# Kernel tuning notes

Measured on AMD Instinct MI355X. Metric: run time of the kernel, lower is better.

## Reference

```python
import jax, jax.numpy as jnp
import numpy as np

N = 200000          # nodes
E = 6400000         # edges (before self-loops)
L = 4               # layer_n
H = 9               # hidden_channels (hardcoded in module)
G = 2000            # graphs in batch
C = 2               # num_classes
NEG_SLOPE = 0.2     # GATConv default leaky_relu slope for attention logits


def setup_inputs() -> dict:
    key = jax.random.key(0)
    ks = jax.random.split(key, 9)
    x = jax.random.normal(ks[0], (N, H), dtype=jnp.float32)
    edge_index = jax.random.randint(ks[1], (2, E), 0, N, dtype=jnp.int32)
    batch = jnp.sort(jax.random.randint(ks[2], (N,), 0, G, dtype=jnp.int32))
    W = jax.random.normal(ks[3], (L, H, H), dtype=jnp.float32) * 0.3
    att_src = jax.random.normal(ks[4], (L, H), dtype=jnp.float32) * 0.3
    att_dst = jax.random.normal(ks[5], (L, H), dtype=jnp.float32) * 0.3
    bias = jax.random.normal(ks[6], (L, H), dtype=jnp.float32) * 0.1
    fc_w = jax.random.normal(ks[7], (L * H, C), dtype=jnp.float32) * 0.2
    fc_b = jax.random.normal(ks[8], (C,), dtype=jnp.float32) * 0.1
    return dict(x=x, edge_index=edge_index, batch=batch, W=W,
                att_src=att_src, att_dst=att_dst, bias=bias,
                fc_w=fc_w, fc_b=fc_b)


def _gat_layer(x, W_l, a_src, a_dst, b_l, src, dst, n):
    # h: [N, H] transformed features (linear, no bias per PyG default)
    h = x @ W_l
    alpha_s = h @ a_src            # [N]
    alpha_d = h @ a_dst            # [N]
    # attention logits per edge (src -> dst), GAT softmax grouped by dst
    e = jax.nn.leaky_relu(alpha_s[src] + alpha_d[dst], NEG_SLOPE)  # [E']
    e = e - jax.ops.segment_max(e, dst, num_segments=n)[dst]
    w = jnp.exp(e)
    denom = jax.ops.segment_sum(w, dst, num_segments=n)[dst]
    alpha = w / denom              # [E']
    out = jax.ops.segment_sum(alpha[:, None] * h[src], dst, num_segments=n)
    return out + b_l


def reference(x, edge_index, batch, W, att_src, att_dst, bias, fc_w, fc_b):
    n = x.shape[0]
    loops = jnp.arange(n, dtype=edge_index.dtype)
    src = jnp.concatenate([edge_index[0], loops])  # add_self_loops=True
    dst = jnp.concatenate([edge_index[1], loops])
    jk = []
    h = x
    for l in range(L):
        h = _gat_layer(h, W[l], att_src[l], att_dst[l], bias[l], src, dst, n)
        h = jax.nn.relu(h)
        jk.append(h)
    jk = jnp.concatenate(jk, axis=1)               # [N, L*H]
    pooled = jax.ops.segment_max(jk, batch, num_segments=G)
    pooled = jnp.where(jnp.isfinite(pooled), pooled, 0.0)  # guard empty graphs
    # dropout is identity at inference
    return pooled @ fc_w + fc_b
```

## Files before the change

### kernel.cpp

```cpp
#include <hip/hip_runtime.h>
#include <hip/hip_fp16.h>

#define Nn 200000
#define Ee 6400000
#define EP 6600000
#define Hh 9
#define Ll 4
#define Gg 2000
#define Cc 2
#define JK 36
#define NCB ((Nn + 1023) >> 10)
#define EPB 8192
#define NBLKA ((EP + EPB - 1) / EPB)
#define NB ((Nn + 255) / 256)
#define NPB 32
#define NAB (Nn / NPB)
#define CAP 3072
#define CAPB 36864
#define HTS (NCB + 1)
#define HALF_N (Nn / 2)

union H2F { __half2 h; float f; };


__global__ __launch_bounds__(256) void kA_scatter(
    const int* __restrict__ src, const int* __restrict__ dst,
    int* __restrict__ ctot, int* __restrict__ histT,
    unsigned* __restrict__ bucketed)
{
    __shared__ unsigned pbuf[EPB];
    __shared__ int lh[NCB];
    __shared__ int s[256];
    int t = threadIdx.x;
    if (t < NCB) lh[t] = 0;
    __syncthreads();
    const int base = blockIdx.x * EPB;
    const int nseg = min(EPB, EP - base);
    for (int j = t; j < nseg; j += 256) {
        int e = base + j;
        int d = (e < Ee) ? dst[e] : (e - Ee);
        atomicAdd(&lh[d >> 10], 1);
    }
    __syncthreads();
    int v = (t < NCB) ? lh[t] : 0;
    s[t] = v; __syncthreads();
    for (int off = 1; off < 256; off <<= 1) {
        int u = (t >= off) ? s[t - off] : 0;
        __syncthreads();
        s[t] += u;
        __syncthreads();
    }
    int* hrow = histT + (size_t)blockIdx.x * HTS;
    if (t < NCB) {
        int ex = s[t] - v;
        lh[t] = ex;
        hrow[t] = ex;
        if (v) atomicAdd(&ctot[t], v);
    }
    if (t == 0) hrow[NCB] = nseg;
    __syncthreads();
    for (int j = t; j < nseg; j += 256) {
        int e = base + j;
        int sv, d;
        if (e < Ee) { sv = src[e]; d = dst[e]; } else { sv = e - Ee; d = sv; }
        int pos = atomicAdd(&lh[d >> 10], 1);
        unsigned p = (unsigned)sv | ((unsigned)(d & 1023) << 18);
        if (sv >= HALF_N) p |= (1u << 28);
        pbuf[pos] = p;
    }
    __syncthreads();
    for (int j = t; j < nseg; j += 256)
        bucketed[base + j] = pbuf[j];
}

__global__ __launch_bounds__(256) void k_scan(
    const int* __restrict__ ctot, int* __restrict__ cbase,
    int* __restrict__ row_ptr)
{
    __shared__ int s[256];
    int t = threadIdx.x;
    int v = (t < NCB) ? ctot[t] : 0;
    s[t] = v; __syncthreads();
    for (int off = 1; off < 256; off <<= 1) {
        int u = (t >= off) ? s[t - off] : 0;
        __syncthreads();
        s[t] += u;
        __syncthreads();
    }
    if (t < NCB) cbase[t] = s[t] - v;
    if (t == 0) { cbase[NCB] = EP; row_ptr[Nn] = EP; }
}

__global__ __launch_bounds__(1024) void kB_csr(
    const unsigned* __restrict__ bucketed, const int* __restrict__ histT,
    const int* __restrict__ cbase, int* __restrict__ row_ptr,
    int* __restrict__ csr_src)
{
    __shared__ int2 hb[NBLKA];
    __shared__ int bh[2048];
    __shared__ unsigned pbuf[CAPB];
    __shared__ int wsum[16];
    const int k = blockIdx.x;
    const int t = threadIdx.x;
    const int w = t >> 6, lane = t & 63;
    bh[t] = 0; bh[t + 1024] = 0;
    for (int j = t; j < NBLKA; j += 1024) {
        const int* hrow = histT + (size_t)j * HTS + k;
        hb[j] = make_int2(hrow[0], hrow[1]);
    }
    __syncthreads();
    for (int b = w; b < NBLKA; b += 16 * 4) {
        int2 es[4]; unsigned ps[4];
#pragma unroll
        for (int u = 0; u < 4; ++u) {
            int bb = b + 16 * u;
            int2 e = (bb < NBLKA) ? hb[bb] : make_int2(0, 0);
            es[u] = e;
            int j = e.x + lane;
            ps[u] = (j < e.y)
                ? __builtin_nontemporal_load(bucketed + (size_t)bb * EPB + j)
                : 0u;
        }
#pragma unroll
        for (int u = 0; u < 4; ++u) {
            int bb = b + 16 * u;
            if (bb >= NBLKA) break;
            int j = es[u].x + lane;
            if (j < es[u].y) {
                unsigned p = ps[u];
                atomicAdd(&bh[(((p >> 18) & 1023) << 1) | ((p >> 28) & 1)], 1);
            }
            for (j += 64; j < es[u].y; j += 64) {
                unsigned p = __builtin_nontemporal_load(
                    bucketed + (size_t)bb * EPB + j);
                atomicAdd(&bh[(((p >> 18) & 1023) << 1) | ((p >> 28) & 1)], 1);
            }
        }
    }
    __syncthreads();
    int v0 = bh[2 * t], v1 = bh[2 * t + 1];
    int sum = v0 + v1;
    int incl = sum;
#pragma unroll
    for (int off = 1; off < 64; off <<= 1) {
        int u = __shfl_up(incl, off);
        if (lane >= off) incl += u;
    }
    if (lane == 63) wsum[w] = incl;
    __syncthreads();
    if (t == 0) {
        int acc = 0;
#pragma unroll
        for (int i2 = 0; i2 < 16; ++i2) { int x = wsum[i2]; wsum[i2] = acc; acc += x; }
    }
    __syncthreads();
    int excl = wsum[w] + incl - sum;
    const int base_k = cbase[k];
    const int nseg_b = cbase[k + 1] - base_k;
    const int node = (k << 10) + t;
    if (node < Nn) row_ptr[node] = base_k + excl;
    bh[2 * t] = excl;
    bh[2 * t + 1] = excl + v0;
    __syncthreads();
    const bool fit = (nseg_b <= CAPB);
    if (fit) {
        for (int b = w; b < NBLKA; b += 16 * 4) {
            int2 es[4]; unsigned ps[4];
#pragma unroll
            for (int u = 0; u < 4; ++u) {
                int bb = b + 16 * u;
                int2 e = (bb < NBLKA) ? hb[bb] : make_int2(0, 0);
                es[u] = e;
                int j = e.x + lane;
                ps[u] = (j < e.y)
                    ? __builtin_nontemporal_load(bucketed + (size_t)bb * EPB + j)
                    : 0u;
            }
#pragma unroll
            for (int u = 0; u < 4; ++u) {
                int bb = b + 16 * u;
                if (bb >= NBLKA) break;
                int j = es[u].x + lane;
                if (j < es[u].y) {
                    unsigned p = ps[u];
                    int pos = atomicAdd(
                        &bh[(((p >> 18) & 1023) << 1) | ((p >> 28) & 1)], 1);
                    pbuf[pos] = p & 0x3FFFFu;
                }
                for (j += 64; j < es[u].y; j += 64) {
                    unsigned p = __builtin_nontemporal_load(
                        bucketed + (size_t)bb * EPB + j);
                    int pos = atomicAdd(
                        &bh[(((p >> 18) & 1023) << 1) | ((p >> 28) & 1)], 1);
                    pbuf[pos] = p & 0x3FFFFu;
                }
            }
        }
        __syncthreads();
        for (int j = t; j < nseg_b; j += 1024)
            csr_src[base_k + j] = (int)pbuf[j];
    } else {
        for (int b = w; b < NBLKA; b += 16) {
            int2 e = hb[b];
            int rb = b * EPB;
            for (int j = e.x + lane; j < e.y; j += 64) {
                unsigned p = bucketed[rb + j];
                int pos = base_k + atomicAdd(
                    &bh[(((p >> 18) & 1023) << 1) | ((p >> 28) & 1)], 1);
                csr_src[pos] = (int)(p & 0x3FFFFu);
            }
        }
    }
}


__global__ __launch_bounds__(256) void k_transform(
    const float* __restrict__ xin, int xstride,
    const float* __restrict__ Wl,
    const float* __restrict__ adst,
    char* __restrict__ P)
{
    int i = blockIdx.x * blockDim.x + threadIdx.x;
    if (i >= Nn) return;
    const float* xp = xin + (size_t)i * xstride;
    float xi[Hh];
#pragma unroll
    for (int k = 0; k < Hh; ++k) xi[k] = xp[k];
    float hv[Hh];
#pragma unroll
    for (int j = 0; j < Hh; ++j) {
        float s = 0.f;
#pragma unroll
        for (int k = 0; k < Hh; ++k) s += xi[k] * Wl[k * Hh + j];
        hv[j] = s;
    }
    float ad = 0.f;
#pragma unroll
    for (int j = 0; j < Hh; ++j) ad += hv[j] * adst[j];
    H2F u01, u23, u45, u67;
    u01.h = __floats2half2_rn(hv[0], hv[1]);
    u23.h = __floats2half2_rn(hv[2], hv[3]);
    u45.h = __floats2half2_rn(hv[4], hv[5]);
    u67.h = __floats2half2_rn(hv[6], hv[7]);
    char* rp = P + ((size_t)i << 5);
    *(float4*)rp        = make_float4(u01.f, u23.f, u45.f, u67.f);
    *(float2*)(rp + 16) = make_float2(hv[8], ad);
}

#define AGG_EDGE(F, X8)                                                     \
    {                                                                       \
        H2F u; float2 p;                                                    \
        u.f = (F).x; p = __half22float2(u.h); float x0 = p.x, x1 = p.y;     \
        u.f = (F).y; p = __half22float2(u.h); float x2 = p.x, x3 = p.y;     \
        u.f = (F).z; p = __half22float2(u.h); float x4 = p.x, x5 = p.y;     \
        u.f = (F).w; p = __half22float2(u.h); float x6 = p.x, x7 = p.y;     \
        float x8 = (X8);                                                    \
        float as = x0*s0 + x1*s1 + x2*s2 + x3*s3 + x4*s4                    \
                 + x5*s5 + x6*s6 + x7*s7 + x8*s8;                           \
        float lg = as + c;                                                  \
        lg = lg > 0.f ? lg : 0.2f * lg;                                     \
        float wgt = __expf(lg);                                             \
        a0 += wgt*x0; a1 += wgt*x1; a2 += wgt*x2; a3 += wgt*x3;             \
        a4 += wgt*x4; a5 += wgt*x5; a6 += wgt*x6; a7 += wgt*x7;             \
        a8 += wgt*x8; den += wgt;                                           \
    }

__global__ __launch_bounds__(256) void k_node_agg(
    const int* __restrict__ rp, const int* __restrict__ csr,
    const char* __restrict__ P, const float* __restrict__ asrc,
    const float* __restrict__ biasl,
    float* __restrict__ jk, int l)
{
    __shared__ int scsr[CAP];
    __shared__ int srp[NPB + 1];
    const int nbase = blockIdx.x * NPB;
    const int t = threadIdx.x;
    if (t <= NPB) srp[t] = rp[nbase + t];
    __syncthreads();
    const int beg_blk = srp[0];
    const int nseg = srp[NPB] - beg_blk;
    const bool use_lds = (nseg <= CAP);
    if (use_lds)
        for (int j = t; j < nseg; j += 256)
            scsr[j] = __builtin_nontemporal_load(csr + beg_blk + j);
    __syncthreads();

    const float s0 = asrc[0], s1 = asrc[1], s2 = asrc[2], s3 = asrc[3],
                s4 = asrc[4], s5 = asrc[5], s6 = asrc[6], s7 = asrc[7],
                s8 = asrc[8];

    const int ni = t >> 3;
    const int q  = t & 7;
    const int i  = nbase + ni;
    const float c = *(const float*)(P + ((size_t)i << 5) + 20);
    float a0=0,a1=0,a2=0,a3=0,a4=0,a5=0,a6=0,a7=0,a8=0,den=0;
    if (use_lds) {
        const int iend = srp[ni + 1] - beg_blk;
        int i0 = srp[ni] - beg_blk + q;
        int i1 = i0 + 8;
        int sv0 = (i0 < iend) ? scsr[i0] : 0;
        int sv1 = (i1 < iend) ? scsr[i1] : 0;
        const char* r0 = P + ((size_t)sv0 << 5);
        const char* r1 = P + ((size_t)sv1 << 5);
        float4 F0 = *(const float4*)r0; float e0 = *(const float*)(r0 + 16);
        float4 F1 = *(const float4*)r1; float e1 = *(const float*)(r1 + 16);
        while (i0 < iend) {
            int n0 = i0 + 16, n1 = i1 + 16;
            int sn0 = (n0 < iend) ? scsr[n0] : 0;
            int sn1 = (n1 < iend) ? scsr[n1] : 0;
            const char* rn0 = P + ((size_t)sn0 << 5);
            const char* rn1 = P + ((size_t)sn1 << 5);
            float4 Fn0 = *(const float4*)rn0;
            float en0 = *(const float*)(rn0 + 16);
            float4 Fn1 = *(const float4*)rn1;
            float en1 = *(const float*)(rn1 + 16);
            AGG_EDGE(F0, e0);
            if (i1 < iend) AGG_EDGE(F1, e1);
            F0 = Fn0; e0 = en0; F1 = Fn1; e1 = en1;
            i0 = n0; i1 = n1;
        }
    } else {
        for (int e = srp[ni] + q; e < srp[ni + 1]; e += 8) {
            int s = csr[e];
            const char* r0 = P + ((size_t)s << 5);
            float4 F = *(const float4*)r0;
            float e8 = *(const float*)(r0 + 16);
            AGG_EDGE(F, e8);
        }
    }
#pragma unroll
    for (int m = 1; m <= 4; m <<= 1) {
        a0 += __shfl_xor(a0, m); a1 += __shfl_xor(a1, m);
        a2 += __shfl_xor(a2, m); a3 += __shfl_xor(a3, m);
        a4 += __shfl_xor(a4, m); a5 += __shfl_xor(a5, m);
        a6 += __shfl_xor(a6, m); a7 += __shfl_xor(a7, m);
        a8 += __shfl_xor(a8, m); den += __shfl_xor(den, m);
    }
    if (q == 0) {
        float inv = 1.f / den;
        float* jp = jk + (size_t)l * Nn * Hh + (size_t)i * Hh;
        jp[0] = fmaxf(a0*inv + biasl[0], 0.f);
        jp[1] = fmaxf(a1*inv + biasl[1], 0.f);
        jp[2] = fmaxf(a2*inv + biasl[2], 0.f);
        jp[3] = fmaxf(a3*inv + biasl[3], 0.f);
        jp[4] = fmaxf(a4*inv + biasl[4], 0.f);
        jp[5] = fmaxf(a5*inv + biasl[5], 0.f);
        jp[6] = fmaxf(a6*inv + biasl[6], 0.f);
        jp[7] = fmaxf(a7*inv + biasl[7], 0.f);
        jp[8] = fmaxf(a8*inv + biasl[8], 0.f);
    }
}


__global__ __launch_bounds__(256) void k_graph_ptr(
    const int* __restrict__ batch, int* __restrict__ gp)
{
    int i = blockIdx.x * 256 + threadIdx.x;
    if (i >= Nn) return;
    int b = batch[i];
    if (i == 0) {
        for (int g = 0; g <= b; ++g) gp[g] = 0;
    } else {
        int pb = batch[i - 1];
        for (int g = pb + 1; g <= b; ++g) gp[g] = i;
    }
    if (i == Nn - 1) {
        for (int g = b + 1; g <= Gg; ++g) gp[g] = Nn;
    }
}

__global__ __launch_bounds__(256) void k_pool_seg(
    const float* __restrict__ jk, const int* __restrict__ gp,
    float* __restrict__ pooled)
{
    int t = blockIdx.x * 256 + threadIdx.x;
    if (t >= Gg * JK) return;
    int g = t / JK, col = t - g * JK;
    int lc = col / Hh, cc = col - lc * Hh;
    const float* bp = jk + (size_t)lc * Nn * Hh + cc;
    int beg = gp[g], end = gp[g + 1];
    float m = 0.f;
    for (int i = beg; i < end; ++i)
        m = fmaxf(m, bp[(size_t)i * Hh]);
    pooled[t] = m;
}

__global__ __launch_bounds__(256) void k_fc(
    const float* __restrict__ pooled, const float* __restrict__ fcw,
    const float* __restrict__ fcb, float* __restrict__ out)
{
    int t = blockIdx.x * blockDim.x + threadIdx.x;
    if (t >= Gg * Cc) return;
    int g = t / Cc, c = t - g * Cc;
    float s = fcb[c];
    const float* pp = pooled + (size_t)g * JK;
#pragma unroll
    for (int j = 0; j < JK; ++j) s += pp[j] * fcw[j * Cc + c];
    out[t] = s;
}

extern "C" void kernel_launch(void* const* d_in, const int* in_sizes, int n_in,
                              void* d_out, int out_size, void* d_ws, size_t ws_size,
                              hipStream_t stream) {
    const float* x      = (const float*)d_in[0];
    const int*   ei     = (const int*)d_in[1];
    const int*   batch  = (const int*)d_in[2];
    const float* W      = (const float*)d_in[3];
    const float* a_src  = (const float*)d_in[4];
    const float* a_dst  = (const float*)d_in[5];
    const float* bias   = (const float*)d_in[6];
    const float* fc_w   = (const float*)d_in[7];
    const float* fc_b   = (const float*)d_in[8];
    float* out = (float*)d_out;

    char* P          = (char*)d_ws;
    float* jk        = (float*)(P + ((size_t)Nn << 5));
    float* pooled    = jk + (size_t)Nn * JK;
    int* row_ptr     = (int*)(pooled + (size_t)Gg * JK);
    int* gp          = row_ptr + Nn + 1;
    int* ctot        = gp + Gg + 1;
    int* cbase       = ctot + NCB;
    int* csr_src     = cbase + NCB + 1;
    int* histT       = (int*)P;
    unsigned* bucketed = (unsigned*)jk;

    const int* srcp = ei;
    const int* dstp = ei + Ee;

    hipMemsetAsync(ctot, 0, NCB * sizeof(int), stream);
    kA_scatter<<<NBLKA, 256, 0, stream>>>(srcp, dstp, ctot, histT, bucketed);
    k_scan    <<<1, 256, 0, stream>>>(ctot, cbase, row_ptr);
    kB_csr    <<<NCB, 1024, 0, stream>>>(bucketed, histT, cbase, row_ptr, csr_src);

    for (int l = 0; l < Ll; ++l) {
        const float* xin = (l == 0) ? x : (jk + (size_t)(l - 1) * Nn * Hh);
        k_transform<<<NB, 256, 0, stream>>>(xin, Hh, W + l * Hh * Hh,
                                            a_dst + l * Hh, P);
        k_node_agg<<<NAB, 256, 0, stream>>>(row_ptr, csr_src, P,
                                            a_src + l * Hh, bias + l * Hh, jk, l);
    }
    k_graph_ptr<<<NB, 256, 0, stream>>>(batch, gp);
    k_pool_seg<<<(Gg * JK + 255) / 256, 256, 0, stream>>>(jk, gp, pooled);
    k_fc<<<(Gg * Cc + 255) / 256, 256, 0, stream>>>(pooled, fc_w, fc_b, out);
}
```

Before: 497.6 us.

## Split CSR by source half and aggregate in two passes for gather locality

The CSR is split into two partitions by source node index (below or above half of N). Each partition gets its own row pointers, so every layer runs the aggregation kernel twice, once per half. The first pass stores partial sums and denominators, and the second pass adds them and applies normalization, bias and ReLU. Gathering from only half of the feature table at a time is meant to improve L2/cache locality, at the cost of an extra kernel launch and an extra jk/den round-trip per layer. The softmax max subtraction is presumably absent or handled elsewhere.

```diff
diff --git a/kernel.cpp b/kernel.cpp
--- a/kernel.cpp
+++ b/kernel.cpp
@@ -18,21 +18,23 @@
 #define CAP 3072
 #define CAPB 36864
 #define HTS (NCB + 1)
-#define HALF_N (Nn / 2)
+#define HALF_N 100000
 
 union H2F { __half2 h; float f; };
 
 
 __global__ __launch_bounds__(256) void kA_scatter(
     const int* __restrict__ src, const int* __restrict__ dst,
-    int* __restrict__ ctot, int* __restrict__ histT,
+    int* __restrict__ ctotH, int* __restrict__ histT,
     unsigned* __restrict__ bucketed)
 {
     __shared__ unsigned pbuf[EPB];
     __shared__ int lh[NCB];
+    __shared__ int lhh[2 * NCB];
     __shared__ int s[256];
     int t = threadIdx.x;
     if (t < NCB) lh[t] = 0;
+    for (int j = t; j < 2 * NCB; j += 256) lhh[j] = 0;
     __syncthreads();
     const int base = blockIdx.x * EPB;
     const int nseg = min(EPB, EP - base);
@@ -55,7 +57,6 @@
         int ex = s[t] - v;
         lh[t] = ex;
         hrow[t] = ex;
-        if (v) atomicAdd(&ctot[t], v);
     }
     if (t == 0) hrow[NCB] = nseg;
     __syncthreads();
@@ -63,43 +64,49 @@
         int e = base + j;
         int sv, d;
         if (e < Ee) { sv = src[e]; d = dst[e]; } else { sv = e - Ee; d = sv; }
+        int hbit = (sv >= HALF_N) ? 1 : 0;
         int pos = atomicAdd(&lh[d >> 10], 1);
-        unsigned p = (unsigned)sv | ((unsigned)(d & 1023) << 18);
-        if (sv >= HALF_N) p |= (1u << 28);
-        pbuf[pos] = p;
+        atomicAdd(&lhh[((d >> 10) << 1) | hbit], 1);
+        pbuf[pos] = (unsigned)sv | ((unsigned)(d & 1023) << 18)
+                  | ((unsigned)hbit << 28);
     }
     __syncthreads();
     for (int j = t; j < nseg; j += 256)
         bucketed[base + j] = pbuf[j];
-}
-
-__global__ __launch_bounds__(256) void k_scan(
-    const int* __restrict__ ctot, int* __restrict__ cbase,
-    int* __restrict__ row_ptr)
-{
-    __shared__ int s[256];
+    for (int j = t; j < 2 * NCB; j += 256) {
+        int c = lhh[j];
+        if (c) atomicAdd(&ctotH[(j & 1) * NCB + (j >> 1)], c);
+    }
+}
+
+__global__ __launch_bounds__(512) void k_scan(
+    const int* __restrict__ ctotH, int* __restrict__ cbaseH,
+    int* __restrict__ rpA, int* __restrict__ rpB)
+{
+    __shared__ int s[512];
     int t = threadIdx.x;
-    int v = (t < NCB) ? ctot[t] : 0;
+    int v = (t < 2 * NCB) ? ctotH[t] : 0;
     s[t] = v; __syncthreads();
-    for (int off = 1; off < 256; off <<= 1) {
+    for (int off = 1; off < 512; off <<= 1) {
         int u = (t >= off) ? s[t - off] : 0;
         __syncthreads();
         s[t] += u;
         __syncthreads();
     }
-    if (t < NCB) cbase[t] = s[t] - v;
-    if (t == 0) { cbase[NCB] = EP; row_ptr[Nn] = EP; }
+    if (t < 2 * NCB) cbaseH[t] = s[t] - v;
+    if (t == NCB) rpA[Nn] = s[NCB] - v;
+    if (t == 0) { cbaseH[2 * NCB] = EP; rpB[Nn] = EP; }
 }
 
 __global__ __launch_bounds__(1024) void kB_csr(
     const unsigned* __restrict__ bucketed, const int* __restrict__ histT,
-    const int* __restrict__ cbase, int* __restrict__ row_ptr,
-    int* __restrict__ csr_src)
+    const int* __restrict__ cbaseH, int* __restrict__ rpA,
+    int* __restrict__ rpB, int* __restrict__ csr_src)
 {
     __shared__ int2 hb[NBLKA];
     __shared__ int bh[2048];
     __shared__ unsigned pbuf[CAPB];
-    __shared__ int wsum[16];
+    __shared__ int wsumA[16], wsumB[16];
     const int k = blockIdx.x;
     const int t = threadIdx.x;
     const int w = t >> 6, lane = t & 63;
@@ -139,28 +146,35 @@
     }
     __syncthreads();
     int v0 = bh[2 * t], v1 = bh[2 * t + 1];
-    int sum = v0 + v1;
-    int incl = sum;
+    int iA = v0, iB = v1;
 #pragma unroll
     for (int off = 1; off < 64; off <<= 1) {
-        int u = __shfl_up(incl, off);
-        if (lane >= off) incl += u;
-    }
-    if (lane == 63) wsum[w] = incl;
+        int uA = __shfl_up(iA, off);
+        int uB = __shfl_up(iB, off);
+        if (lane >= off) { iA += uA; iB += uB; }
+    }
+    if (lane == 63) { wsumA[w] = iA; wsumB[w] = iB; }
     __syncthreads();
     if (t == 0) {
         int acc = 0;
 #pragma unroll
-        for (int i2 = 0; i2 < 16; ++i2) { int x = wsum[i2]; wsum[i2] = acc; acc += x; }
-    }
-    __syncthreads();
-    int excl = wsum[w] + incl - sum;
-    const int base_k = cbase[k];
-    const int nseg_b = cbase[k + 1] - base_k;
+        for (int i2 = 0; i2 < 16; ++i2) { int x = wsumA[i2]; wsumA[i2] = acc; acc += x; }
+        acc = 0;
+#pragma unroll
+        for (int i2 = 0; i2 < 16; ++i2) { int x = wsumB[i2]; wsumB[i2] = acc; acc += x; }
+    }
+    __syncthreads();
+    int exA = wsumA[w] + iA - v0;
+    int exB = wsumB[w] + iB - v1;
+    const int baseA = cbaseH[k];
+    const int totA  = cbaseH[k + 1] - baseA;
+    const int baseB = cbaseH[NCB + k];
+    const int totB  = cbaseH[NCB + k + 1] - baseB;
+    const int nseg_b = totA + totB;
     const int node = (k << 10) + t;
-    if (node < Nn) row_ptr[node] = base_k + excl;
-    bh[2 * t] = excl;
-    bh[2 * t + 1] = excl + v0;
+    if (node < Nn) { rpA[node] = baseA + exA; rpB[node] = baseB + exB; }
+    bh[2 * t] = exA;
+    bh[2 * t + 1] = totA + exB;
     __syncthreads();
     const bool fit = (nseg_b <= CAPB);
     if (fit) {
@@ -197,17 +211,20 @@
             }
         }
         __syncthreads();
-        for (int j = t; j < nseg_b; j += 1024)
-            csr_src[base_k + j] = (int)pbuf[j];
+        for (int j = t; j < totA; j += 1024)
+            csr_src[baseA + j] = (int)pbuf[j];
+        for (int j = t; j < totB; j += 1024)
+            csr_src[baseB + j] = (int)pbuf[totA + j];
     } else {
         for (int b = w; b < NBLKA; b += 16) {
             int2 e = hb[b];
             int rb = b * EPB;
             for (int j = e.x + lane; j < e.y; j += 64) {
                 unsigned p = bucketed[rb + j];
-                int pos = base_k + atomicAdd(
+                int pos = atomicAdd(
                     &bh[(((p >> 18) & 1023) << 1) | ((p >> 28) & 1)], 1);
-                csr_src[pos] = (int)(p & 0x3FFFFu);
+                int abspos = (pos < totA) ? baseA + pos : baseB + (pos - totA);
+                csr_src[abspos] = (int)(p & 0x3FFFFu);
             }
         }
     }
@@ -269,7 +286,7 @@
     const int* __restrict__ rp, const int* __restrict__ csr,
     const char* __restrict__ P, const float* __restrict__ asrc,
     const float* __restrict__ biasl,
-    float* __restrict__ jk, int l)
+    float* __restrict__ jk, float* __restrict__ denP, int l, int mode)
 {
     __shared__ int scsr[CAP];
     __shared__ int srp[NPB + 1];
@@ -337,17 +354,26 @@
         a8 += __shfl_xor(a8, m); den += __shfl_xor(den, m);
     }
     if (q == 0) {
-        float inv = 1.f / den;
         float* jp = jk + (size_t)l * Nn * Hh + (size_t)i * Hh;
-        jp[0] = fmaxf(a0*inv + biasl[0], 0.f);
-        jp[1] = fmaxf(a1*inv + biasl[1], 0.f);
-        jp[2] = fmaxf(a2*inv + biasl[2], 0.f);
-        jp[3] = fmaxf(a3*inv + biasl[3], 0.f);
-        jp[4] = fmaxf(a4*inv + biasl[4], 0.f);
-        jp[5] = fmaxf(a5*inv + biasl[5], 0.f);
-        jp[6] = fmaxf(a6*inv + biasl[6], 0.f);
-        jp[7] = fmaxf(a7*inv + biasl[7], 0.f);
-        jp[8] = fmaxf(a8*inv + biasl[8], 0.f);
+        if (mode == 0) {
+            jp[0] = a0; jp[1] = a1; jp[2] = a2; jp[3] = a3; jp[4] = a4;
+            jp[5] = a5; jp[6] = a6; jp[7] = a7; jp[8] = a8;
+            denP[i] = den;
+        } else {
+            a0 += jp[0]; a1 += jp[1]; a2 += jp[2]; a3 += jp[3]; a4 += jp[4];
+            a5 += jp[5]; a6 += jp[6]; a7 += jp[7]; a8 += jp[8];
+            den += denP[i];
+            float inv = 1.f / den;
+            jp[0] = fmaxf(a0*inv + biasl[0], 0.f);
+            jp[1] = fmaxf(a1*inv + biasl[1], 0.f);
+            jp[2] = fmaxf(a2*inv + biasl[2], 0.f);
+            jp[3] = fmaxf(a3*inv + biasl[3], 0.f);
+            jp[4] = fmaxf(a4*inv + biasl[4], 0.f);
+            jp[5] = fmaxf(a5*inv + biasl[5], 0.f);
+            jp[6] = fmaxf(a6*inv + biasl[6], 0.f);
+            jp[7] = fmaxf(a7*inv + biasl[7], 0.f);
+            jp[8] = fmaxf(a8*inv + biasl[8], 0.f);
+        }
     }
 }
 
@@ -416,28 +442,33 @@
     char* P          = (char*)d_ws;
     float* jk        = (float*)(P + ((size_t)Nn << 5));
     float* pooled    = jk + (size_t)Nn * JK;
-    int* row_ptr     = (int*)(pooled + (size_t)Gg * JK);
-    int* gp          = row_ptr + Nn + 1;
-    int* ctot        = gp + Gg + 1;
-    int* cbase       = ctot + NCB;
-    int* csr_src     = cbase + NCB + 1;
+    int* rpA         = (int*)(pooled + (size_t)Gg * JK);
+    int* rpB         = rpA + Nn + 1;
+    int* gp          = rpB + Nn + 1;
+    int* ctotH       = gp + Gg + 1;
+    int* cbaseH      = ctotH + 2 * NCB;
+    float* denP      = (float*)(cbaseH + 2 * NCB + 1);
+    int* csr_src     = (int*)(denP + Nn);
     int* histT       = (int*)P;
     unsigned* bucketed = (unsigned*)jk;
 
     const int* srcp = ei;
     const int* dstp = ei + Ee;
 
-    hipMemsetAsync(ctot, 0, NCB * sizeof(int), stream);
-    kA_scatter<<<NBLKA, 256, 0, stream>>>(srcp, dstp, ctot, histT, bucketed);
-    k_scan    <<<1, 256, 0, stream>>>(ctot, cbase, row_ptr);
-    kB_csr    <<<NCB, 1024, 0, stream>>>(bucketed, histT, cbase, row_ptr, csr_src);
+    hipMemsetAsync(ctotH, 0, 2 * NCB * sizeof(int), stream);
+    kA_scatter<<<NBLKA, 256, 0, stream>>>(srcp, dstp, ctotH, histT, bucketed);
+    k_scan    <<<1, 512, 0, stream>>>(ctotH, cbaseH, rpA, rpB);
+    kB_csr    <<<NCB, 1024, 0, stream>>>(bucketed, histT, cbaseH, rpA, rpB,
+                                         csr_src);
 
     for (int l = 0; l < Ll; ++l) {
         const float* xin = (l == 0) ? x : (jk + (size_t)(l - 1) * Nn * Hh);
         k_transform<<<NB, 256, 0, stream>>>(xin, Hh, W + l * Hh * Hh,
                                             a_dst + l * Hh, P);
-        k_node_agg<<<NAB, 256, 0, stream>>>(row_ptr, csr_src, P,
-                                            a_src + l * Hh, bias + l * Hh, jk, l);
+        k_node_agg<<<NAB, 256, 0, stream>>>(rpA, csr_src, P, a_src + l * Hh,
+                                            bias + l * Hh, jk, denP, l, 0);
+        k_node_agg<<<NAB, 256, 0, stream>>>(rpB, csr_src, P, a_src + l * Hh,
+                                            bias + l * Hh, jk, denP, l, 1);
     }
     k_graph_ptr<<<NB, 256, 0, stream>>>(batch, gp);
     k_pool_seg<<<(Gg * JK + 255) / 256, 256, 0, stream>>>(jk, gp, pooled);
```

After: 496.9 us. Within noise of the previous version (-0.1%).
